# Performance work log

Hardware: AMD Instinct MI355X
Metric: run time of the kernel (lower is better)

The kernel has to match this reference:

```python
import jax, jax.numpy as jnp
import numpy as np

B, S, D, H = 4, 2048, 1024, 16
HD = D // H

def setup_inputs() -> dict:
    key = jax.random.key(0)
    ks = jax.random.split(key, 11)
    s = 1.0 / np.sqrt(D)
    return {
        "query": jax.random.normal(ks[0], (B, S, D), jnp.float32),
        "key_": jax.random.normal(ks[1], (B, S, D), jnp.float32),
        "value": jax.random.normal(ks[2], (B, S, D), jnp.float32),
        "Wq": jax.random.normal(ks[3], (D, D), jnp.float32) * s,
        "bq": jax.random.normal(ks[4], (D,), jnp.float32) * s,
        "Wk": jax.random.normal(ks[5], (D, D), jnp.float32) * s,
        "bk": jax.random.normal(ks[6], (D,), jnp.float32) * s,
        "Wv": jax.random.normal(ks[7], (D, D), jnp.float32) * s,
        "bv": jax.random.normal(ks[8], (D,), jnp.float32) * s,
        "Wo": jax.random.normal(ks[9], (D, D), jnp.float32) * s,
        "bo": jax.random.normal(ks[10], (D,), jnp.float32) * s,
    }

def reference(query, key_, value, Wq, bq, Wk, bk, Wv, bv, Wo, bo):
    # projections (torch Linear: x @ W.T + b)
    q = query @ Wq.T + bq
    k = key_ @ Wk.T + bk
    v = value @ Wv.T + bv
    # [B,S,D] -> [B,H,S,hd]
    q = q.reshape(B, S, H, HD).transpose(0, 2, 1, 3)
    k = k.reshape(B, S, H, HD).transpose(0, 2, 1, 3)
    v = v.reshape(B, S, H, HD).transpose(0, 2, 1, 3)
    scale = HD ** 0.5
    scores = jnp.einsum('bhqd,bhkd->bhqk', q, k) / scale
    attn = jax.nn.softmax(scores, axis=-1)
    out = jnp.einsum('bhqk,bhkd->bhqd', attn, v)
    out = out.transpose(0, 2, 1, 3).reshape(B, S, D)
    return out @ Wo.T + bo
```

## Files before the change

### kernel.cpp

```cpp
#include <hip/hip_runtime.h>
#include <math.h>

#define B_ 4
#define S_ 2048
#define D_ 1024
#define H_ 16
#define HD_ 64
#define M_ (B_*S_)
#define BH_ (B_*H_)

typedef __attribute__((ext_vector_type(4))) float f32x4;
typedef _Float16 f16;
typedef __attribute__((ext_vector_type(8))) _Float16 f16x8;
typedef __attribute__((ext_vector_type(2))) __fp16 fp16x2_raw;
typedef unsigned short u16;

#define QSCALE 0.18033688011112042f

__device__ __forceinline__ unsigned pkh(float a, float b) {
    fp16x2_raw h = __builtin_amdgcn_cvt_pkrtz(a, b);
    unsigned r; __builtin_memcpy(&r, &h, 4);
    return r;
}
__device__ __forceinline__ uint2 f4_to_h4(float4 v) {
    uint2 r;
    r.x = pkh(v.x, v.y);
    r.y = pkh(v.z, v.w);
    return r;
}
__device__ __forceinline__ void gload_lds16(const void* g, void* l) {
    __builtin_amdgcn_global_load_lds(
        (const __attribute__((address_space(1))) void*)g,
        (__attribute__((address_space(3))) void*)l, 16, 0, 0);
}
#define MFMA16(a,b,c) __builtin_amdgcn_mfma_f32_16x16x32_f16((a),(b),(c),0,0,0)

__global__ __launch_bounds__(256) void conv_w_kernel(
    const float* __restrict__ w0, const float* __restrict__ w1,
    const float* __restrict__ w2, const float* __restrict__ w3,
    f16* __restrict__ out)
{
    const float* src = (blockIdx.y==0)?w0:(blockIdx.y==1)?w1:(blockIdx.y==2)?w2:w3;
    size_t off = (size_t)blockIdx.y << 20;
    size_t i = ((size_t)blockIdx.x*256 + threadIdx.x)*4;
    float4 v = *(const float4*)&src[i];
    *(uint2*)&out[off + i] = f4_to_h4(v);
}

__global__ __launch_bounds__(256) void conv_in_kernel(
    const float* __restrict__ src, f16* __restrict__ out)
{
    size_t i = ((size_t)blockIdx.x*256 + threadIdx.x)*4;
    float4 v = *(const float4*)&src[i];
    *(uint2*)&out[i] = f4_to_h4(v);
}

template<int MODE>
__global__ __launch_bounds__(256, 2) void gemm_mfma(
    const f16* __restrict__ Af16,
    const f16* __restrict__ Wh16,
    const float* __restrict__ bias,
    void* out0)
{
    __shared__ u16 Ah[128][32];
    __shared__ u16 Bh[128][32];

    const int t = threadIdx.x;
    const int lane = t & 63;
    const int w = t >> 6;
    const int wm = w >> 1, wn = w & 1;
    const int m0 = (int)(blockIdx.x >> 3) * 128;
    const int n0 = (int)(blockIdx.x & 7) * 128;

    const int srow_base = w*32;
    const int lrow_off  = lane >> 2;
    const int k8        = (lane & 3) * 8;

    f32x4 acc[4][4];
    #pragma unroll
    for (int i = 0; i < 4; ++i)
        #pragma unroll
        for (int j = 0; j < 4; ++j) { f32x4 z = {0.f,0.f,0.f,0.f}; acc[i][j] = z; }

    for (int k0 = 0; k0 < D_; k0 += 32) {
        __syncthreads();
        #pragma unroll
        for (int c = 0; c < 2; ++c) {
            int lrow = srow_base + c*16;
            int row = lrow + lrow_off;
            int kw = k8 ^ ((row & 3) << 3);
            size_t asrc;
            if constexpr (MODE == 3) {
                int m = m0 + row;
                int b = m >> 11, s = m & 2047;
                int kk = k0 + kw;
                asrc = (((size_t)b*H_ + (kk >> 6))*S_ + s)*HD_ + (kk & 63);
            } else {
                asrc = (size_t)(m0 + row)*D_ + k0 + kw;
            }
            gload_lds16(&Af16[asrc], &Ah[lrow][0]);
            gload_lds16(&Wh16[(size_t)(n0 + row)*D_ + k0 + kw], &Bh[lrow][0]);
        }
        __syncthreads();

        f16x8 ah[4], bh4[4];
        #pragma unroll
        for (int i = 0; i < 4; ++i) {
            int ml = wm*64 + i*16 + (lane & 15);
            int kwa = ((lane >> 4) * 8) ^ ((ml & 3) << 3);
            ah[i] = *(const f16x8*)&Ah[ml][kwa];
            int nl = wn*64 + i*16 + (lane & 15);
            int kwb = ((lane >> 4) * 8) ^ ((nl & 3) << 3);
            bh4[i] = *(const f16x8*)&Bh[nl][kwb];
        }
        __builtin_amdgcn_s_setprio(1);
        #pragma unroll
        for (int i = 0; i < 4; ++i)
            #pragma unroll
            for (int j = 0; j < 4; ++j)
                acc[i][j] = MFMA16(ah[i], bh4[j], acc[i][j]);
        __builtin_amdgcn_s_setprio(0);
    }

    #pragma unroll
    for (int i = 0; i < 4; ++i) {
        #pragma unroll
        for (int j = 0; j < 4; ++j) {
            int n = n0 + wn*64 + j*16 + (lane & 15);
            float bb = bias[n];
            int mbase = m0 + wm*64 + i*16 + (lane >> 4)*4;
            if constexpr (MODE == 3) {
                float* o = (float*)out0;
                #pragma unroll
                for (int r = 0; r < 4; ++r)
                    o[(size_t)(mbase + r)*D_ + n] = acc[i][j][r] + bb;
            } else if constexpr (MODE == 0) {
                f16* q = (f16*)out0;
                int b = mbase >> 11, h = n >> 6, hd = n & 63;
                size_t bh = (size_t)b*H_ + h;
                #pragma unroll
                for (int r = 0; r < 4; ++r) {
                    int s = (mbase + r) & 2047;
                    q[(bh*S_ + s)*64 + hd] = (f16)((acc[i][j][r] + bb) * QSCALE);
                }
            } else if constexpr (MODE == 1) {
                f16* oh = (f16*)out0;
                int b = mbase >> 11, h = n >> 6, hd = n & 63;
                size_t bh = (size_t)b*H_ + h;
                #pragma unroll
                for (int r = 0; r < 4; ++r) {
                    int s = (mbase + r) & 2047;
                    oh[(bh*S_ + s)*64 + hd] = (f16)(acc[i][j][r] + bb);
                }
            } else {
                int b = mbase >> 11, h = n >> 6, hd = n & 63;
                int s0 = mbase & 2047;
                uint2 ph;
                ph.x = pkh(acc[i][j][0] + bb, acc[i][j][1] + bb);
                ph.y = pkh(acc[i][j][2] + bb, acc[i][j][3] + bb);
                size_t idx = (((size_t)b*H_ + h)*HD_ + hd)*S_ + s0;
                *(uint2*)&((f16*)out0)[idx] = ph;
            }
        }
    }
}

__global__ __launch_bounds__(256, 2) void attn_mfma(
    const f16* __restrict__ kf,
    const f16* __restrict__ vtf,
    f16* qf)
{
    __shared__ u16 Kh[2][64][64];
    __shared__ u16 Vth[2][64][64];
    __shared__ u16 Ps[256][64];

    const int t = threadIdx.x;
    const int lane = t & 63;
    const int w = t >> 6;
    const int g = lane >> 4;
    const int l15 = lane & 15;

    const int lb = (int)blockIdx.x;
    const int logical = (lb & 7) * 64 + (lb >> 3);
    const int qtile = logical & 7;
    const int bh = logical >> 3;
    const size_t rowb = (size_t)bh * S_;
    const int q0 = qtile * 256;

    const int srow_off = lane >> 3;
    const int sd8      = (lane & 7) * 8;

    f16x8 qh[4][2];
    {
        int qr = q0 + w*64 + l15;
        #pragma unroll
        for (int mi = 0; mi < 4; ++mi)
            #pragma unroll
            for (int kk = 0; kk < 2; ++kk) {
                int d0 = kk*32 + g*8;
                qh[mi][kk] = *(const f16x8*)&qf[(rowb + qr + mi*16)*64 + d0];
            }
    }

    const f32x4 zero4 = {0.f, 0.f, 0.f, 0.f};
    f16x8 ones8;
    #pragma unroll
    for (int e = 0; e < 8; ++e) ones8[e] = (f16)1.0f;

    f32x4 O[4][4];
    f32x4 lacc[4];
    #pragma unroll
    for (int mi = 0; mi < 4; ++mi) {
        lacc[mi] = zero4;
        #pragma unroll
        for (int oj = 0; oj < 4; ++oj) O[mi][oj] = zero4;
    }

#define STAGE_KV(bsel, kt_) do { \
        _Pragma("unroll") \
        for (int c = 0; c < 2; ++c) { \
            int lrow = w*16 + c*8; \
            int row = lrow + srow_off; \
            int dsw = sd8 ^ ((row & 7) << 3); \
            size_t kg = (rowb + (kt_)*64 + row)*64 + dsw; \
            size_t vg = ((size_t)bh*HD_ + row)*S_ + (kt_)*64 + dsw; \
            gload_lds16(&kf[kg],  &Kh[bsel][lrow][0]); \
            gload_lds16(&vtf[vg], &Vth[bsel][lrow][0]); \
        } \
    } while (0)

    STAGE_KV(0, 0);

    const int NT = S_/64;
    for (int kt = 0; kt < NT; ++kt) {
        const int cur = kt & 1;
        if (kt + 1 < NT) {
            STAGE_KV(cur ^ 1, kt + 1);
            asm volatile("s_waitcnt vmcnt(4)" ::: "memory");
        } else {
            asm volatile("s_waitcnt vmcnt(0)" ::: "memory");
        }
        __builtin_amdgcn_s_barrier();

        f32x4 sa[4][4];
        {
            f16x8 kb[4];
            #pragma unroll
            for (int k4 = 0; k4 < 4; ++k4) {
                int kv = k4*16 + l15;
                int dw = (g*8) ^ ((kv & 7) << 3);
                kb[k4] = *(const f16x8*)&Kh[cur][kv][dw];
            }
            __builtin_amdgcn_s_setprio(1);
            #pragma unroll
            for (int k4 = 0; k4 < 4; ++k4)
                #pragma unroll
                for (int qt = 0; qt < 4; ++qt)
                    sa[k4][qt] = MFMA16(kb[k4], qh[qt][0], zero4);
            __builtin_amdgcn_s_setprio(0);
        }
        {
            f16x8 kb[4];
            #pragma unroll
            for (int k4 = 0; k4 < 4; ++k4) {
                int kv = k4*16 + l15;
                int dw = (32 + g*8) ^ ((kv & 7) << 3);
                kb[k4] = *(const f16x8*)&Kh[cur][kv][dw];
            }
            __builtin_amdgcn_s_setprio(1);
            #pragma unroll
            for (int k4 = 0; k4 < 4; ++k4)
                #pragma unroll
                for (int qt = 0; qt < 4; ++qt)
                    sa[k4][qt] = MFMA16(kb[k4], qh[qt][1], sa[k4][qt]);
            __builtin_amdgcn_s_setprio(0);
        }

        u16* Pflat = &Ps[0][0];
        #pragma unroll
        for (int qt = 0; qt < 4; ++qt) {
            int qw = w*64 + qt*16 + l15;
            int prow = qw * 64;
            int sw = (qw & 7) << 3;
            #pragma unroll
            for (int k4 = 0; k4 < 4; ++k4) {
                float p0 = exp2f(sa[k4][qt][0]);
                float p1 = exp2f(sa[k4][qt][1]);
                float p2 = exp2f(sa[k4][qt][2]);
                float p3 = exp2f(sa[k4][qt][3]);
                uint2 pk;
                pk.x = pkh(p0, p1);
                pk.y = pkh(p2, p3);
                int kvb = k4*16 + g*4;
                *(uint2*)&Pflat[prow + (kvb ^ sw)] = pk;
            }
        }

        #pragma unroll
        for (int k2 = 0; k2 < 2; ++k2) {
            f16x8 pa[4], vb[4];
            #pragma unroll
            for (int mi = 0; mi < 4; ++mi) {
                int q = w*64 + mi*16 + l15;
                int kw = (k2*32 + g*8) ^ ((q & 7) << 3);
                pa[mi] = *(const f16x8*)&Pflat[q*64 + kw];
            }
            #pragma unroll
            for (int oj = 0; oj < 4; ++oj) {
                int hd = oj*16 + l15;
                int kw = (k2*32 + g*8) ^ ((hd & 7) << 3);
                vb[oj] = *(const f16x8*)&Vth[cur][hd][kw];
            }
            __builtin_amdgcn_s_setprio(1);
            #pragma unroll
            for (int mi = 0; mi < 4; ++mi) {
                #pragma unroll
                for (int oj = 0; oj < 4; ++oj)
                    O[mi][oj] = MFMA16(pa[mi], vb[oj], O[mi][oj]);
                lacc[mi] = MFMA16(pa[mi], ones8, lacc[mi]);
            }
            __builtin_amdgcn_s_setprio(0);
        }

        __builtin_amdgcn_s_barrier();
    }
#undef STAGE_KV

    #pragma unroll
    for (int mi = 0; mi < 4; ++mi)
        #pragma unroll
        for (int r = 0; r < 4; ++r) {
            float iv = 1.f / lacc[mi][r];
            int q = q0 + w*64 + mi*16 + g*4 + r;
            #pragma unroll
            for (int oj = 0; oj < 4; ++oj) {
                int hd = oj*16 + l15;
                qf[(rowb + q)*HD_ + hd] = (f16)(O[mi][oj][r] * iv);
            }
        }
}

extern "C" void kernel_launch(void* const* d_in, const int* in_sizes, int n_in,
                              void* d_out, int out_size, void* d_ws, size_t ws_size,
                              hipStream_t stream) {
    const float* query = (const float*)d_in[0];
    const float* key_  = (const float*)d_in[1];
    const float* value = (const float*)d_in[2];
    const float* Wq    = (const float*)d_in[3];
    const float* bq    = (const float*)d_in[4];
    const float* Wk    = (const float*)d_in[5];
    const float* bk    = (const float*)d_in[6];
    const float* Wv    = (const float*)d_in[7];
    const float* bv    = (const float*)d_in[8];
    const float* Wo    = (const float*)d_in[9];
    const float* bo    = (const float*)d_in[10];
    float* out = (float*)d_out;

    char* wsb = (char*)d_ws;
    const size_t SZ_H = (size_t)BH_*S_*64*2;
    f16* qf   = (f16*)wsb;
    f16* kf   = (f16*)(wsb + SZ_H);
    f16* vtf  = (f16*)(wsb + 2*SZ_H);
    f16* in16 = (f16*)(wsb + 3*SZ_H);
    f16* W16  = (f16*)(wsb + 4*SZ_H);

    dim3 gGemm(512);
    dim3 gAttn(512);
    dim3 gConv(8192);

    conv_w_kernel<<<dim3(1024,4), 256, 0, stream>>>(Wq, Wk, Wv, Wo, W16);
    conv_in_kernel<<<gConv, 256, 0, stream>>>(query, in16);
    gemm_mfma<0><<<gGemm, 256, 0, stream>>>(in16, W16 + ((size_t)0<<20), bq, qf);
    conv_in_kernel<<<gConv, 256, 0, stream>>>(key_, in16);
    gemm_mfma<1><<<gGemm, 256, 0, stream>>>(in16, W16 + ((size_t)1<<20), bk, kf);
    conv_in_kernel<<<gConv, 256, 0, stream>>>(value, in16);
    gemm_mfma<2><<<gGemm, 256, 0, stream>>>(in16, W16 + ((size_t)2<<20), bv, vtf);
    attn_mfma<<<gAttn, 256, 0, stream>>>(kf, vtf, qf);
    gemm_mfma<3><<<gGemm, 256, 0, stream>>>(qf, W16 + ((size_t)3<<20), bo, out);
}
```

Measured before the change: 248.8 us.

## Software-pipeline QK^T of next tile with softmax of current tile

Restructures the attention main loop so the QK^T MFMAs for key tile kt+1 are interleaved with the exp2/pack of tile kt. K and V loads are staged separately, with K prefetched two tiles ahead and V one tile ahead, and two score register buffers are ping-ponged across a 2x unrolled loop. The goal is to overlap transcendental/VALU softmax work with matrix-core work. The cost is doubled score registers (32 extra f32x4), which may raise register pressure and lower occupancy.

```diff
diff --git a/kernel.cpp b/kernel.cpp
--- a/kernel.cpp
+++ b/kernel.cpp
@@ -216,115 +216,124 @@
         for (int oj = 0; oj < 4; ++oj) O[mi][oj] = zero4;
     }
 
-#define STAGE_KV(bsel, kt_) do { \
+    const int NT = S_/64;
+
+#define STAGE_K(bsel, kt_) do { \
         _Pragma("unroll") \
         for (int c = 0; c < 2; ++c) { \
             int lrow = w*16 + c*8; \
             int row = lrow + srow_off; \
             int dsw = sd8 ^ ((row & 7) << 3); \
-            size_t kg = (rowb + (kt_)*64 + row)*64 + dsw; \
-            size_t vg = ((size_t)bh*HD_ + row)*S_ + (kt_)*64 + dsw; \
-            gload_lds16(&kf[kg],  &Kh[bsel][lrow][0]); \
-            gload_lds16(&vtf[vg], &Vth[bsel][lrow][0]); \
-        } \
-    } while (0)
-
-    STAGE_KV(0, 0);
-
-    const int NT = S_/64;
-    for (int kt = 0; kt < NT; ++kt) {
-        const int cur = kt & 1;
-        if (kt + 1 < NT) {
-            STAGE_KV(cur ^ 1, kt + 1);
-            asm volatile("s_waitcnt vmcnt(4)" ::: "memory");
-        } else {
-            asm volatile("s_waitcnt vmcnt(0)" ::: "memory");
-        }
-        __builtin_amdgcn_s_barrier();
-
-        f32x4 sa[4][4];
-        {
-            f16x8 kb[4];
-            #pragma unroll
-            for (int k4 = 0; k4 < 4; ++k4) {
-                int kv = k4*16 + l15;
-                int dw = (g*8) ^ ((kv & 7) << 3);
-                kb[k4] = *(const f16x8*)&Kh[cur][kv][dw];
-            }
-            __builtin_amdgcn_s_setprio(1);
-            #pragma unroll
-            for (int k4 = 0; k4 < 4; ++k4)
-                #pragma unroll
-                for (int qt = 0; qt < 4; ++qt)
-                    sa[k4][qt] = MFMA16(kb[k4], qh[qt][0], zero4);
-            __builtin_amdgcn_s_setprio(0);
-        }
-        {
-            f16x8 kb[4];
-            #pragma unroll
-            for (int k4 = 0; k4 < 4; ++k4) {
-                int kv = k4*16 + l15;
-                int dw = (32 + g*8) ^ ((kv & 7) << 3);
-                kb[k4] = *(const f16x8*)&Kh[cur][kv][dw];
-            }
-            __builtin_amdgcn_s_setprio(1);
-            #pragma unroll
-            for (int k4 = 0; k4 < 4; ++k4)
-                #pragma unroll
-                for (int qt = 0; qt < 4; ++qt)
-                    sa[k4][qt] = MFMA16(kb[k4], qh[qt][1], sa[k4][qt]);
-            __builtin_amdgcn_s_setprio(0);
-        }
-
-        u16* Pflat = &Ps[0][0];
-        #pragma unroll
-        for (int qt = 0; qt < 4; ++qt) {
-            int qw = w*64 + qt*16 + l15;
-            int prow = qw * 64;
-            int sw = (qw & 7) << 3;
-            #pragma unroll
-            for (int k4 = 0; k4 < 4; ++k4) {
-                float p0 = exp2f(sa[k4][qt][0]);
-                float p1 = exp2f(sa[k4][qt][1]);
-                float p2 = exp2f(sa[k4][qt][2]);
-                float p3 = exp2f(sa[k4][qt][3]);
-                uint2 pk;
-                pk.x = pkh(p0, p1);
-                pk.y = pkh(p2, p3);
-                int kvb = k4*16 + g*4;
-                *(uint2*)&Pflat[prow + (kvb ^ sw)] = pk;
-            }
-        }
-
-        #pragma unroll
-        for (int k2 = 0; k2 < 2; ++k2) {
-            f16x8 pa[4], vb[4];
-            #pragma unroll
-            for (int mi = 0; mi < 4; ++mi) {
-                int q = w*64 + mi*16 + l15;
-                int kw = (k2*32 + g*8) ^ ((q & 7) << 3);
-                pa[mi] = *(const f16x8*)&Pflat[q*64 + kw];
-            }
-            #pragma unroll
-            for (int oj = 0; oj < 4; ++oj) {
-                int hd = oj*16 + l15;
-                int kw = (k2*32 + g*8) ^ ((hd & 7) << 3);
-                vb[oj] = *(const f16x8*)&Vth[cur][hd][kw];
-            }
-            __builtin_amdgcn_s_setprio(1);
-            #pragma unroll
-            for (int mi = 0; mi < 4; ++mi) {
-                #pragma unroll
-                for (int oj = 0; oj < 4; ++oj)
-                    O[mi][oj] = MFMA16(pa[mi], vb[oj], O[mi][oj]);
-                lacc[mi] = MFMA16(pa[mi], ones8, lacc[mi]);
-            }
-            __builtin_amdgcn_s_setprio(0);
-        }
-
-        __builtin_amdgcn_s_barrier();
-    }
-#undef STAGE_KV
+            gload_lds16(&kf[(rowb + (kt_)*64 + row)*64 + dsw], &Kh[bsel][lrow][0]); \
+        } \
+    } while (0)
+#define STAGE_V(bsel, kt_) do { \
+        _Pragma("unroll") \
+        for (int c = 0; c < 2; ++c) { \
+            int lrow = w*16 + c*8; \
+            int row = lrow + srow_off; \
+            int dsw = sd8 ^ ((row & 7) << 3); \
+            gload_lds16(&vtf[((size_t)bh*HD_ + row)*S_ + (kt_)*64 + dsw], &Vth[bsel][lrow][0]); \
+        } \
+    } while (0)
+
+#define QK_SLICE(SA, KSEL, k4) do { \
+        int kv = (k4)*16 + l15; \
+        int dw0 = (g*8)      ^ ((kv & 7) << 3); \
+        int dw1 = (32 + g*8) ^ ((kv & 7) << 3); \
+        f16x8 kb0 = *(const f16x8*)&Kh[KSEL][kv][dw0]; \
+        f16x8 kb1 = *(const f16x8*)&Kh[KSEL][kv][dw1]; \
+        _Pragma("unroll") \
+        for (int qt = 0; qt < 4; ++qt) { \
+            SA[(k4)][qt] = MFMA16(kb0, qh[qt][0], zero4); \
+            SA[(k4)][qt] = MFMA16(kb1, qh[qt][1], SA[(k4)][qt]); \
+        } \
+    } while (0)
+
+#define SM_SLICE(SA, k4) do { \
+        _Pragma("unroll") \
+        for (int qt = 0; qt < 4; ++qt) { \
+            int qw = w*64 + qt*16 + l15; \
+            int prow = qw * 64; \
+            int sw = (qw & 7) << 3; \
+            float p0 = exp2f(SA[(k4)][qt][0]); \
+            float p1 = exp2f(SA[(k4)][qt][1]); \
+            float p2 = exp2f(SA[(k4)][qt][2]); \
+            float p3 = exp2f(SA[(k4)][qt][3]); \
+            uint2 pk; \
+            pk.x = pkh(p0, p1); \
+            pk.y = pkh(p2, p3); \
+            int kvb = (k4)*16 + g*4; \
+            *(uint2*)&(&Ps[0][0])[prow + (kvb ^ sw)] = pk; \
+        } \
+    } while (0)
+
+#define ITER(SA_CUR, SA_NEXT, kt_) do { \
+        const int cb = (kt_) & 1; \
+        if ((kt_)+2 < NT) STAGE_K(cb, (kt_)+2); \
+        if ((kt_)+1 < NT) STAGE_V(cb^1, (kt_)+1); \
+        if ((kt_)+2 < NT)      asm volatile("s_waitcnt vmcnt(4)" ::: "memory"); \
+        else if ((kt_)+1 < NT) asm volatile("s_waitcnt vmcnt(2)" ::: "memory"); \
+        else                   asm volatile("s_waitcnt vmcnt(0)" ::: "memory"); \
+        __builtin_amdgcn_s_barrier(); \
+        if ((kt_)+1 < NT) { \
+            _Pragma("unroll") \
+            for (int k4 = 0; k4 < 4; ++k4) { \
+                QK_SLICE(SA_NEXT, cb^1, k4); \
+                SM_SLICE(SA_CUR, k4); \
+            } \
+        } else { \
+            _Pragma("unroll") \
+            for (int k4 = 0; k4 < 4; ++k4) SM_SLICE(SA_CUR, k4); \
+        } \
+         \
+        _Pragma("unroll") \
+        for (int k2 = 0; k2 < 2; ++k2) { \
+            f16x8 pa[4], vb[4]; \
+            _Pragma("unroll") \
+            for (int mi = 0; mi < 4; ++mi) { \
+                int q = w*64 + mi*16 + l15; \
+                int kw = (k2*32 + g*8) ^ ((q & 7) << 3); \
+                pa[mi] = *(const f16x8*)&(&Ps[0][0])[q*64 + kw]; \
+            } \
+            _Pragma("unroll") \
+            for (int oj = 0; oj < 4; ++oj) { \
+                int hd = oj*16 + l15; \
+                int kw = (k2*32 + g*8) ^ ((hd & 7) << 3); \
+                vb[oj] = *(const f16x8*)&Vth[cb][hd][kw]; \
+            } \
+            __builtin_amdgcn_s_setprio(1); \
+            _Pragma("unroll") \
+            for (int mi = 0; mi < 4; ++mi) { \
+                _Pragma("unroll") \
+                for (int oj = 0; oj < 4; ++oj) \
+                    O[mi][oj] = MFMA16(pa[mi], vb[oj], O[mi][oj]); \
+                lacc[mi] = MFMA16(pa[mi], ones8, lacc[mi]); \
+            } \
+            __builtin_amdgcn_s_setprio(0); \
+        } \
+        __builtin_amdgcn_s_barrier(); \
+    } while (0)
+
+    f32x4 saA[4][4], saB[4][4];
+    STAGE_K(0, 0);
+    STAGE_V(0, 0);
+    STAGE_K(1, 1);
+    asm volatile("s_waitcnt vmcnt(4)" ::: "memory");
+    __builtin_amdgcn_s_barrier();
+    #pragma unroll
+    for (int k4 = 0; k4 < 4; ++k4) QK_SLICE(saA, 0, k4);
+    __builtin_amdgcn_s_barrier();
+
+    for (int kt = 0; kt < NT; kt += 2) {
+        ITER(saA, saB, kt);
+        ITER(saB, saA, kt + 1);
+    }
+#undef ITER
+#undef SM_SLICE
+#undef QK_SLICE
+#undef STAGE_V
+#undef STAGE_K
 
     #pragma unroll
     for (int mi = 0; mi < 4; ++mi)
```

Result: slower. 374.1 us (+50.4%).
